# Optimization experiments

Measured on AMD Instinct MI355X. Metric: run time of the kernel, lower is better.

Reference implementation:

```python
import jax, jax.numpy as jnp
import numpy as np

# Config matching init_kwargs (single TP rank: local heads == total heads)
HID = 1024
NH = 16      # query heads
NKV = 4      # kv heads (GQA)
HD = 64      # head_dim
B = 2
S = 2048
SCALE = 1.0 / HD ** 0.5


def setup_inputs() -> dict:
    key = jax.random.key(0)
    k1, k2, k3 = jax.random.split(key, 3)
    qkv_out = (NH + 2 * NKV) * HD  # 1536
    return {
        "hidden_states": jax.random.normal(k1, (B, S, HID), dtype=jnp.float32),
        "W_qkv": jax.random.normal(k2, (HID, qkv_out), dtype=jnp.float32) * 0.02,
        "W_o": jax.random.normal(k3, (HID, HID), dtype=jnp.float32) * 0.02,
    }


def reference(hidden_states, W_qkv, W_o):
    b, s, _ = hidden_states.shape
    rep = NH // NKV  # GQA repeat factor (repeat_interleave: q head h uses kv group h // rep)

    qkv = hidden_states @ W_qkv  # [B, S, (NH+2*NKV)*HD]
    q, k, v = jnp.split(qkv, [NH * HD, (NH + NKV) * HD], axis=-1)

    # [B, heads, S, HD]
    q = q.reshape(b, s, NH, HD).transpose(0, 2, 1, 3)
    k = k.reshape(b, s, NKV, HD).transpose(0, 2, 1, 3)
    v = v.reshape(b, s, NKV, HD).transpose(0, 2, 1, 3)

    # Group query heads by shared kv head instead of repeat_interleaving K/V in memory.
    qg = q.reshape(b, NKV, rep, s, HD)  # head h = g*rep + r  <=>  kv group g = h // rep
    scores = jnp.einsum("bgrqd,bgkd->bgrqk", qg, k) * SCALE  # [B, NKV, rep, S, S]

    # Causal mask (prefill path: kv_cache is None, seq_len > 1)
    causal = jnp.triu(jnp.ones((s, s), dtype=bool), k=1)
    scores = jnp.where(causal, jnp.finfo(scores.dtype).min, scores)

    attn = jax.nn.softmax(scores, axis=-1)
    out = jnp.einsum("bgrqk,bgkd->bgrqd", attn, v)  # [B, NKV, rep, S, HD]
    out = out.reshape(b, NH, s, HD).transpose(0, 2, 1, 3).reshape(b, s, NH * HD)
    return out @ W_o  # [B, S, HID]
```

## Files before the change

### kernel.cpp

```cpp
#include <hip/hip_runtime.h>
#include <stdint.h>

using u16 = unsigned short;
using u32 = unsigned int;

typedef __attribute__((ext_vector_type(8))) short short8;
typedef __attribute__((ext_vector_type(4))) float f32x4;
typedef __attribute__((ext_vector_type(16))) float f32x16;

__device__ __forceinline__ u16 f2bf(float f) {
  u32 u = __builtin_bit_cast(u32, f);
  u = (u + 0x7fffu + ((u >> 16) & 1u)) >> 16;
  return (u16)u;
}

__device__ __forceinline__ u32 cvtpk(float lo, float hi) {
  u32 r;
  asm("v_cvt_pk_bf16_f32 %0, %1, %2" : "=v"(r) : "v"(lo), "v"(hi));
  return r;
}

__device__ __forceinline__ short8 ld16(const u16* p) {
  uint4 v = *(const uint4*)p;
  union { uint4 u; short8 s; } c; c.u = v; return c.s;
}

__device__ __forceinline__ void gload_lds16(const void* g, void* l) {
  __builtin_amdgcn_global_load_lds(
      (const __attribute__((address_space(1))) void*)g,
      (__attribute__((address_space(3))) void*)l, 16, 0, 0);
}

__device__ __forceinline__ f32x16 mfma32(short8 a, short8 b, f32x16 c) {
  return __builtin_amdgcn_mfma_f32_32x32x16_bf16(a, b, c, 0, 0, 0);
}

__global__ __launch_bounds__(256) void k_prep(const float* __restrict__ hs,
                                              const float* __restrict__ wqkv,
                                              const float* __restrict__ wo,
                                              u16* __restrict__ hsb,
                                              u16* __restrict__ wqkvT,
                                              u16* __restrict__ woT) {
  __shared__ float tile[32][33];
  const int bid = blockIdx.x;
  if (bid < 4096) {
    int i = bid * 256 + threadIdx.x;
    float4 v = ((const float4*)hs)[i];
    ushort4 o;
    o.x = f2bf(v.x); o.y = f2bf(v.y); o.z = f2bf(v.z); o.w = f2bf(v.w);
    ((ushort4*)hsb)[i] = o;
    return;
  }
  const float* in; u16* out; int R, C, bx, by;
  if (bid < 5632) {
    int idx = bid - 4096;
    in = wqkv; out = wqkvT; R = 1024; C = 1536;
    bx = idx % 48; by = idx / 48;
  } else {
    int idx = bid - 5632;
    in = wo; out = woT; R = 1024; C = 1024;
    bx = idx & 31; by = idx >> 5;
  }
  int c0 = bx * 32, r0 = by * 32;
  int tx = threadIdx.x & 31, ty = threadIdx.x >> 5;
#pragma unroll
  for (int i = 0; i < 4; ++i) {
    int r = ty + 8 * i;
    tile[r][tx] = in[(size_t)(r0 + r) * C + c0 + tx];
  }
  __syncthreads();
#pragma unroll
  for (int i = 0; i < 4; ++i) {
    int r = ty + 8 * i;
    out[(size_t)(c0 + r) * R + r0 + tx] = f2bf(tile[tx][r]);
  }
}

__global__ __launch_bounds__(256, 2) void k_gemm_qkv(
    const u16* __restrict__ A, const u16* __restrict__ BT,
    u16* __restrict__ qb, u16* __restrict__ kb, u16* __restrict__ vbT) {
  const int K = 1024, N = 1536;
  __shared__ __align__(16) u16 As[2][128 * 64];
  __shared__ __align__(16) u16 Bs[2][128 * 64];
  const int t = threadIdx.x;
  const int l = t & 63;
  const int wid = t >> 6;
  const int wr = wid >> 1, wc = wid & 1;
  const int lr = l & 15, lg = l >> 4;
  const int cpx = (int)gridDim.x >> 3;
  const int nb = (blockIdx.x & 7) * cpx + ((int)blockIdx.x >> 3);
  const int ntile = N >> 7;
  const int mt = nb / ntile, nt = nb % ntile;
  const int m0 = mt << 7, n0 = nt << 7;

  f32x4 zero = {0.f, 0.f, 0.f, 0.f};
  f32x4 acc[4][4];
#pragma unroll
  for (int i = 0; i < 4; ++i)
#pragma unroll
    for (int j = 0; j < 4; ++j) acc[i][j] = zero;

  const u16* Ab = A + (size_t)m0 * K;
  const u16* Bb = BT + (size_t)n0 * K;
  const int nkt = K >> 6;

  auto STAGE = [&](int kt, int bsel) {
    const u16* Ak = Ab + kt * 64;
    const u16* Bk = Bb + kt * 64;
#pragma unroll
    for (int i = 0; i < 4; ++i) {
      int o16 = i * 256 + t;
      int row = o16 >> 3, c = o16 & 7;
      int sc = c ^ (row & 7);
      gload_lds16(Ak + (size_t)row * K + sc * 8, &As[bsel][o16 * 8]);
    }
#pragma unroll
    for (int i = 0; i < 4; ++i) {
      int o16 = i * 256 + t;
      int row = o16 >> 3, c = o16 & 7;
      int sc = c ^ (row & 7);
      gload_lds16(Bk + (size_t)row * K + sc * 8, &Bs[bsel][o16 * 8]);
    }
  };

  STAGE(0, 0);
  asm volatile("s_waitcnt vmcnt(0)" ::: "memory");
  __builtin_amdgcn_s_barrier();

  for (int kt = 0; kt < nkt; ++kt) {
    const int cur = kt & 1;
    if (kt + 1 < nkt) STAGE(kt + 1, cur ^ 1);
#pragma unroll
    for (int ks = 0; ks < 2; ++ks) {
      short8 a[4], b[4];
#pragma unroll
      for (int mi = 0; mi < 4; ++mi) {
        int row = wr * 64 + mi * 16 + lr;
        int c = (ks * 4 + lg) ^ (row & 7);
        a[mi] = ld16(&As[cur][(row * 8 + c) * 8]);
      }
#pragma unroll
      for (int ni = 0; ni < 4; ++ni) {
        int row = wc * 64 + ni * 16 + lr;
        int c = (ks * 4 + lg) ^ (row & 7);
        b[ni] = ld16(&Bs[cur][(row * 8 + c) * 8]);
      }
#pragma unroll
      for (int mi = 0; mi < 4; ++mi)
#pragma unroll
        for (int ni = 0; ni < 4; ++ni)
          acc[mi][ni] = __builtin_amdgcn_mfma_f32_16x16x32_bf16(a[mi], b[ni], acc[mi][ni], 0, 0, 0);
    }
    asm volatile("s_waitcnt vmcnt(0)" ::: "memory");
    __builtin_amdgcn_s_barrier();
    asm volatile("" ::: "memory");
  }

#pragma unroll
  for (int mi = 0; mi < 4; ++mi) {
#pragma unroll
    for (int ni = 0; ni < 4; ++ni) {
#pragma unroll
      for (int r = 0; r < 4; ++r) {
        float v = acc[mi][ni][r];
        int m = m0 + wr * 64 + mi * 16 + 4 * lg + r;
        int n = n0 + wc * 64 + ni * 16 + lr;
        int bb = m >> 11, s = m & 2047;
        int tau = s >> 5, i32e = s & 31;
        if (n < 1024) {
          int h = n >> 6, d = n & 63;
          int kc = d >> 4, hi2 = (d >> 3) & 1, e = d & 7;
          qb[((size_t)(bb * 16 + h)) * 131072 +
             (size_t)((tau * 4 + kc) * 64 + (hi2 << 5 | i32e)) * 8 + e] = f2bf(v * 0.18033688f);
        } else if (n < 1280) {
          int g = (n - 1024) >> 6, d = n & 63;
          int kc = d >> 4, hi2 = (d >> 3) & 1, e = d & 7;
          kb[((size_t)(bb * 4 + g)) * 131072 +
             (size_t)((tau * 4 + kc) * 64 + (hi2 << 5 | i32e)) * 8 + e] = f2bf(v);
        } else {
          int g = (n - 1280) >> 6, dT = n & 63;
          int c = (s >> 4) & 1, hi2 = (s >> 3) & 1, e = s & 7;
          int dd = dT >> 5, i32v = dT & 31;
          vbT[((size_t)(bb * 4 + g)) * 131072 +
              (size_t)(((tau * 2 + dd) * 2 + c) * 64 + (hi2 << 5 | i32v)) * 8 + e] = f2bf(v);
        }
      }
    }
  }
}

__global__ __launch_bounds__(256, 2) void k_gemm_out(
    const u16* __restrict__ A, const u16* __restrict__ BT, float* __restrict__ out) {
  const int K = 1024, N = 1024;
  __shared__ __align__(16) u16 As[2][64 * 64];
  __shared__ __align__(16) u16 Bs[2][128 * 64];
  const int t = threadIdx.x;
  const int l = t & 63;
  const int wid = t >> 6;
  const int wr = wid >> 1, wc = wid & 1;
  const int lr = l & 15, lg = l >> 4;
  const int cpx = (int)gridDim.x >> 3;
  const int nb = (blockIdx.x & 7) * cpx + ((int)blockIdx.x >> 3);
  const int mt = nb >> 3, nt = nb & 7;
  const int m0 = mt << 6, n0 = nt << 7;

  f32x4 zero = {0.f, 0.f, 0.f, 0.f};
  f32x4 acc[2][4];
#pragma unroll
  for (int i = 0; i < 2; ++i)
#pragma unroll
    for (int j = 0; j < 4; ++j) acc[i][j] = zero;

  const u16* Ab = A + (size_t)m0 * K;
  const u16* Bb = BT + (size_t)n0 * K;

  auto STAGE = [&](int kt, int bsel) {
    const u16* Ak = Ab + kt * 64;
    const u16* Bk = Bb + kt * 64;
#pragma unroll
    for (int i = 0; i < 2; ++i) {
      int o16 = i * 256 + t;
      int row = o16 >> 3, c = o16 & 7;
      int sc = c ^ (row & 7);
      gload_lds16(Ak + (size_t)row * K + sc * 8, &As[bsel][o16 * 8]);
    }
#pragma unroll
    for (int i = 0; i < 4; ++i) {
      int o16 = i * 256 + t;
      int row = o16 >> 3, c = o16 & 7;
      int sc = c ^ (row & 7);
      gload_lds16(Bk + (size_t)row * K + sc * 8, &Bs[bsel][o16 * 8]);
    }
  };

  STAGE(0, 0);
  asm volatile("s_waitcnt vmcnt(0)" ::: "memory");
  __builtin_amdgcn_s_barrier();

  for (int kt = 0; kt < 16; ++kt) {
    const int cur = kt & 1;
    if (kt + 1 < 16) STAGE(kt + 1, cur ^ 1);
#pragma unroll
    for (int ks = 0; ks < 2; ++ks) {
      short8 a[2], b[4];
#pragma unroll
      for (int mi = 0; mi < 2; ++mi) {
        int row = wr * 32 + mi * 16 + lr;
        int c = (ks * 4 + lg) ^ (row & 7);
        a[mi] = ld16(&As[cur][(row * 8 + c) * 8]);
      }
#pragma unroll
      for (int ni = 0; ni < 4; ++ni) {
        int row = wc * 64 + ni * 16 + lr;
        int c = (ks * 4 + lg) ^ (row & 7);
        b[ni] = ld16(&Bs[cur][(row * 8 + c) * 8]);
      }
#pragma unroll
      for (int mi = 0; mi < 2; ++mi)
#pragma unroll
        for (int ni = 0; ni < 4; ++ni)
          acc[mi][ni] = __builtin_amdgcn_mfma_f32_16x16x32_bf16(a[mi], b[ni], acc[mi][ni], 0, 0, 0);
    }
    asm volatile("s_waitcnt vmcnt(0)" ::: "memory");
    __builtin_amdgcn_s_barrier();
    asm volatile("" ::: "memory");
  }

#pragma unroll
  for (int mi = 0; mi < 2; ++mi)
#pragma unroll
    for (int ni = 0; ni < 4; ++ni)
#pragma unroll
      for (int r = 0; r < 4; ++r) {
        int m = m0 + wr * 32 + mi * 16 + 4 * lg + r;
        int n = n0 + wc * 64 + ni * 16 + lr;
        out[(size_t)m * N + n] = acc[mi][ni][r];
      }
}

__global__ __launch_bounds__(256, 2) void k_attn(const u16* __restrict__ qbuf,
                                                 const u16* __restrict__ kbuf,
                                                 const u16* __restrict__ vbuf,
                                                 u16* __restrict__ attn) {
  const int t = threadIdx.x;
  const int l = t & 63, wid = t >> 6;
  const int i32 = l & 31, hi = l >> 5;
  const int bh = blockIdx.x >> 4;
  const int t16 = blockIdx.x & 15;
  const int b = bh >> 4, h = bh & 15, g = h >> 2;
  const int qt = (wid == 0) ? t16 : (wid == 1) ? 31 - t16 : (wid == 2) ? 32 + t16 : 63 - t16;
  const int q0 = qt * 32;
  const int nblk = (q0 >> 6) + 1;

  const u16* qp = qbuf + ((size_t)(b * 16 + h)) * 131072;
  const u16* kp = kbuf + ((size_t)(b * 4 + g)) * 131072;
  const u16* vp = vbuf + ((size_t)(b * 4 + g)) * 131072;

  short8 qf[4];
#pragma unroll
  for (int kc = 0; kc < 4; ++kc)
    qf[kc] = ld16(qp + ((size_t)((q0 >> 5) * 4 + kc) * 64 + l) * 8);

  f32x16 z16 = {0.f, 0.f, 0.f, 0.f, 0.f, 0.f, 0.f, 0.f,
                0.f, 0.f, 0.f, 0.f, 0.f, 0.f, 0.f, 0.f};
  f32x16 o[2];
  o[0] = z16; o[1] = z16;
  float lsum = 0.f;

  short8 kA[2][4], kB[2][4];

  auto LOADK = [&](short8(&kf)[2][4], int kv0) {
#pragma unroll
    for (int mf = 0; mf < 2; ++mf)
#pragma unroll
      for (int kc = 0; kc < 4; ++kc)
        kf[mf][kc] = ld16(kp + ((size_t)((((kv0 >> 5) + mf) * 4 + kc)) * 64 + l) * 8);
  };

  auto PROCESS = [&](short8(&kf)[2][4], short8(&kn)[2][4], bool pref, int kv0, bool last) {
    short8 vf[2][2][2];
#pragma unroll
    for (int mf = 0; mf < 2; ++mf)
#pragma unroll
      for (int dd = 0; dd < 2; ++dd)
#pragma unroll
        for (int c = 0; c < 2; ++c)
          vf[dd][mf][c] = ld16(vp + ((size_t)((((kv0 >> 5) + mf) * 2 + dd) * 2 + c) * 64 + l) * 8);

    f32x16 sc[2];
    __builtin_amdgcn_s_setprio(1);
    sc[0] = mfma32(kf[0][0], qf[0], z16);
    sc[1] = mfma32(kf[1][0], qf[0], z16);
#pragma unroll
    for (int kc = 1; kc < 4; ++kc) {
      sc[0] = mfma32(kf[0][kc], qf[kc], sc[0]);
      sc[1] = mfma32(kf[1][kc], qf[kc], sc[1]);
    }
    __builtin_amdgcn_s_setprio(0);

    if (pref) LOADK(kn, kv0 + 64);

    if (last) {
      const int iloc = (q0 - kv0) + i32;
#pragma unroll
      for (int mf = 0; mf < 2; ++mf)
#pragma unroll
        for (int R = 0; R < 16; ++R) {
          int j = 32 * mf + (R & 3) + 8 * (R >> 2) + 4 * hi;
          if (j > iloc) sc[mf][R] = -1e30f;
        }
    }

    float s0 = 0.f, s1 = 0.f, s2 = 0.f, s3 = 0.f;
#pragma unroll
    for (int mf = 0; mf < 2; ++mf)
#pragma unroll
      for (int R = 0; R < 16; R += 4) {
        float p0 = __builtin_amdgcn_exp2f(sc[mf][R]);
        float p1 = __builtin_amdgcn_exp2f(sc[mf][R + 1]);
        float p2 = __builtin_amdgcn_exp2f(sc[mf][R + 2]);
        float p3 = __builtin_amdgcn_exp2f(sc[mf][R + 3]);
        sc[mf][R] = p0; sc[mf][R + 1] = p1; sc[mf][R + 2] = p2; sc[mf][R + 3] = p3;
        s0 += p0; s1 += p1; s2 += p2; s3 += p3;
      }
    lsum += (s0 + s1) + (s2 + s3);

    short8 pb[2][2];
#pragma unroll
    for (int mf = 0; mf < 2; ++mf)
#pragma unroll
      for (int c = 0; c < 2; ++c) {
        union { u32 w[4]; short8 s8; } U;
#pragma unroll
        for (int q = 0; q < 2; ++q) {
          u32 wa = cvtpk(sc[mf][8 * c + 2 * q], sc[mf][8 * c + 2 * q + 1]);
          u32 wb = cvtpk(sc[mf][8 * c + 4 + 2 * q], sc[mf][8 * c + 4 + 2 * q + 1]);
          auto rr = __builtin_amdgcn_permlane32_swap(wa, wb, false, false);
          U.w[q] = (u32)rr[0];
          U.w[2 + q] = (u32)rr[1];
        }
        pb[mf][c] = U.s8;
      }

    __builtin_amdgcn_s_setprio(1);
#pragma unroll
    for (int mf = 0; mf < 2; ++mf)
#pragma unroll
      for (int c = 0; c < 2; ++c) {
        o[0] = mfma32(vf[0][mf][c], pb[mf][c], o[0]);
        o[1] = mfma32(vf[1][mf][c], pb[mf][c], o[1]);
      }
    __builtin_amdgcn_s_setprio(0);
  };

  LOADK(kA, 0);
  int kv0 = 0, blk = 0;
  while (true) {
    PROCESS(kA, kB, blk + 1 < nblk, kv0, blk == nblk - 1);
    ++blk; kv0 += 64;
    if (blk >= nblk) break;
    PROCESS(kB, kA, blk + 1 < nblk, kv0, blk == nblk - 1);
    ++blk; kv0 += 64;
    if (blk >= nblk) break;
  }

  float tot;
  {
    u32 su = __builtin_bit_cast(u32, lsum);
    auto rr = __builtin_amdgcn_permlane32_swap(su, su, false, false);
    tot = __builtin_bit_cast(float, (u32)rr[0]) + __builtin_bit_cast(float, (u32)rr[1]);
  }
  float inv = 1.f / tot;
  u16* ao = attn + ((size_t)(b * 2048 + q0)) * 1024 + h * 64;
#pragma unroll
  for (int dd = 0; dd < 2; ++dd) {
#pragma unroll
    for (int R = 0; R < 16; R += 2) {
      int d = dd * 32 + (R & 3) + 8 * (R >> 2) + 4 * hi;
      u32 w = cvtpk(o[dd][R] * inv, o[dd][R + 1] * inv);
      *(u32*)(ao + (size_t)i32 * 1024 + d) = w;
    }
  }
}

extern "C" void kernel_launch(void* const* d_in, const int* in_sizes, int n_in,
                              void* d_out, int out_size, void* d_ws, size_t ws_size,
                              hipStream_t stream) {
  const float* hs = (const float*)d_in[0];
  const float* wqkv = (const float*)d_in[1];
  const float* wo = (const float*)d_in[2];
  float* out = (float*)d_out;
  u16* ws = (u16*)d_ws;

  u16* hsb = ws;
  u16* wqkvT = hsb + 4194304;
  u16* woT = wqkvT + 1572864;
  u16* qb = woT + 1048576;
  u16* kb = qb + 4194304;
  u16* vb = kb + 1048576;
  u16* attn = vb + 1048576;
  (void)in_sizes; (void)n_in; (void)out_size; (void)ws_size;

  k_prep<<<6656, 256, 0, stream>>>(hs, wqkv, wo, hsb, wqkvT, woT);
  k_gemm_qkv<<<384, 256, 0, stream>>>(hsb, wqkvT, qb, kb, vb);
  k_attn<<<512, 256, 0, stream>>>(qb, kb, vb, attn);
  k_gemm_out<<<512, 256, 0, stream>>>(attn, woT, out);
}
```

Baseline: 85.14 us.

## Split attention KV range across waves and shrink QKV GEMM tiles

The attention kernel now assigns one 32-row query tile per block and splits its KV blocks across the four waves in strides of four. Partial outputs and row sums are combined through shared memory before the final normalize and store. This works without max-rescaling because the scores are unnormalized exp2 with no running max. The QKV GEMM halves its M tile to 64 so it launches twice as many blocks, and both kernels raise the occupancy hint to 3. The aim is better load balance and more blocks across CUs, at the cost of extra LDS traffic, a block barrier, and less per-block reuse in the GEMM.

```diff
diff --git a/kernel.cpp b/kernel.cpp
--- a/kernel.cpp
+++ b/kernel.cpp
@@ -76,11 +76,11 @@
   }
 }
 
-__global__ __launch_bounds__(256, 2) void k_gemm_qkv(
+__global__ __launch_bounds__(256, 3) void k_gemm_qkv(
     const u16* __restrict__ A, const u16* __restrict__ BT,
     u16* __restrict__ qb, u16* __restrict__ kb, u16* __restrict__ vbT) {
-  const int K = 1024, N = 1536;
-  __shared__ __align__(16) u16 As[2][128 * 64];
+  const int K = 1024;
+  __shared__ __align__(16) u16 As[2][64 * 64];
   __shared__ __align__(16) u16 Bs[2][128 * 64];
   const int t = threadIdx.x;
   const int l = t & 63;
@@ -89,26 +89,24 @@
   const int lr = l & 15, lg = l >> 4;
   const int cpx = (int)gridDim.x >> 3;
   const int nb = (blockIdx.x & 7) * cpx + ((int)blockIdx.x >> 3);
-  const int ntile = N >> 7;
-  const int mt = nb / ntile, nt = nb % ntile;
-  const int m0 = mt << 7, n0 = nt << 7;
+  const int mt = nb / 12, nt = nb % 12;
+  const int m0 = mt << 6, n0 = nt << 7;
 
   f32x4 zero = {0.f, 0.f, 0.f, 0.f};
-  f32x4 acc[4][4];
-#pragma unroll
-  for (int i = 0; i < 4; ++i)
+  f32x4 acc[2][4];
+#pragma unroll
+  for (int i = 0; i < 2; ++i)
 #pragma unroll
     for (int j = 0; j < 4; ++j) acc[i][j] = zero;
 
   const u16* Ab = A + (size_t)m0 * K;
   const u16* Bb = BT + (size_t)n0 * K;
-  const int nkt = K >> 6;
 
   auto STAGE = [&](int kt, int bsel) {
     const u16* Ak = Ab + kt * 64;
     const u16* Bk = Bb + kt * 64;
 #pragma unroll
-    for (int i = 0; i < 4; ++i) {
+    for (int i = 0; i < 2; ++i) {
       int o16 = i * 256 + t;
       int row = o16 >> 3, c = o16 & 7;
       int sc = c ^ (row & 7);
@@ -127,15 +125,15 @@
   asm volatile("s_waitcnt vmcnt(0)" ::: "memory");
   __builtin_amdgcn_s_barrier();
 
-  for (int kt = 0; kt < nkt; ++kt) {
+  for (int kt = 0; kt < 16; ++kt) {
     const int cur = kt & 1;
-    if (kt + 1 < nkt) STAGE(kt + 1, cur ^ 1);
+    if (kt + 1 < 16) STAGE(kt + 1, cur ^ 1);
 #pragma unroll
     for (int ks = 0; ks < 2; ++ks) {
-      short8 a[4], b[4];
-#pragma unroll
-      for (int mi = 0; mi < 4; ++mi) {
-        int row = wr * 64 + mi * 16 + lr;
+      short8 a[2], b[4];
+#pragma unroll
+      for (int mi = 0; mi < 2; ++mi) {
+        int row = wr * 32 + mi * 16 + lr;
         int c = (ks * 4 + lg) ^ (row & 7);
         a[mi] = ld16(&As[cur][(row * 8 + c) * 8]);
       }
@@ -146,7 +144,7 @@
         b[ni] = ld16(&Bs[cur][(row * 8 + c) * 8]);
       }
 #pragma unroll
-      for (int mi = 0; mi < 4; ++mi)
+      for (int mi = 0; mi < 2; ++mi)
 #pragma unroll
         for (int ni = 0; ni < 4; ++ni)
           acc[mi][ni] = __builtin_amdgcn_mfma_f32_16x16x32_bf16(a[mi], b[ni], acc[mi][ni], 0, 0, 0);
@@ -157,13 +155,13 @@
   }
 
 #pragma unroll
-  for (int mi = 0; mi < 4; ++mi) {
+  for (int mi = 0; mi < 2; ++mi) {
 #pragma unroll
     for (int ni = 0; ni < 4; ++ni) {
 #pragma unroll
       for (int r = 0; r < 4; ++r) {
         float v = acc[mi][ni][r];
-        int m = m0 + wr * 64 + mi * 16 + 4 * lg + r;
+        int m = m0 + wr * 32 + mi * 16 + 4 * lg + r;
         int n = n0 + wc * 64 + ni * 16 + lr;
         int bb = m >> 11, s = m & 2047;
         int tau = s >> 5, i32e = s & 31;
@@ -278,19 +276,20 @@
       }
 }
 
-__global__ __launch_bounds__(256, 2) void k_attn(const u16* __restrict__ qbuf,
+__global__ __launch_bounds__(256, 3) void k_attn(const u16* __restrict__ qbuf,
                                                  const u16* __restrict__ kbuf,
                                                  const u16* __restrict__ vbuf,
                                                  u16* __restrict__ attn) {
+  __shared__ float oshare[3 * 2048];
+  __shared__ float lshare[3 * 64];
   const int t = threadIdx.x;
   const int l = t & 63, wid = t >> 6;
   const int i32 = l & 31, hi = l >> 5;
-  const int bh = blockIdx.x >> 4;
-  const int t16 = blockIdx.x & 15;
+  const int bh = blockIdx.x >> 6;
+  const int qt = blockIdx.x & 63;
   const int b = bh >> 4, h = bh & 15, g = h >> 2;
-  const int qt = (wid == 0) ? t16 : (wid == 1) ? 31 - t16 : (wid == 2) ? 32 + t16 : 63 - t16;
   const int q0 = qt * 32;
-  const int nblk = (q0 >> 6) + 1;
+  const int nblk = (qt >> 1) + 1;
 
   const u16* qp = qbuf + ((size_t)(b * 16 + h)) * 131072;
   const u16* kp = kbuf + ((size_t)(b * 4 + g)) * 131072;
@@ -338,7 +337,7 @@
     }
     __builtin_amdgcn_s_setprio(0);
 
-    if (pref) LOADK(kn, kv0 + 64);
+    if (pref) LOADK(kn, kv0 + 256);
 
     if (last) {
       const int iloc = (q0 - kv0) + i32;
@@ -393,32 +392,64 @@
     __builtin_amdgcn_s_setprio(0);
   };
 
-  LOADK(kA, 0);
-  int kv0 = 0, blk = 0;
-  while (true) {
-    PROCESS(kA, kB, blk + 1 < nblk, kv0, blk == nblk - 1);
-    ++blk; kv0 += 64;
-    if (blk >= nblk) break;
-    PROCESS(kB, kA, blk + 1 < nblk, kv0, blk == nblk - 1);
-    ++blk; kv0 += 64;
-    if (blk >= nblk) break;
-  }
-
-  float tot;
-  {
-    u32 su = __builtin_bit_cast(u32, lsum);
-    auto rr = __builtin_amdgcn_permlane32_swap(su, su, false, false);
-    tot = __builtin_bit_cast(float, (u32)rr[0]) + __builtin_bit_cast(float, (u32)rr[1]);
-  }
-  float inv = 1.f / tot;
-  u16* ao = attn + ((size_t)(b * 2048 + q0)) * 1024 + h * 64;
-#pragma unroll
-  for (int dd = 0; dd < 2; ++dd) {
-#pragma unroll
-    for (int R = 0; R < 16; R += 2) {
-      int d = dd * 32 + (R & 3) + 8 * (R >> 2) + 4 * hi;
-      u32 w = cvtpk(o[dd][R] * inv, o[dd][R + 1] * inv);
-      *(u32*)(ao + (size_t)i32 * 1024 + d) = w;
+  if (wid < nblk) {
+    LOADK(kA, wid * 64);
+    int n = wid;
+    while (true) {
+      PROCESS(kA, kB, n + 4 < nblk, n * 64, n == nblk - 1);
+      n += 4; if (n >= nblk) break;
+      PROCESS(kB, kA, n + 4 < nblk, n * 64, n == nblk - 1);
+      n += 4; if (n >= nblk) break;
+    }
+  }
+
+  if (wid > 0) {
+    const int base = (wid - 1) * 2048;
+#pragma unroll
+    for (int dd = 0; dd < 2; ++dd) {
+      float4* dst = (float4*)&oshare[base + (dd * 64 + l) * 16];
+#pragma unroll
+      for (int q = 0; q < 4; ++q) {
+        float4 v4;
+        v4.x = o[dd][4 * q]; v4.y = o[dd][4 * q + 1];
+        v4.z = o[dd][4 * q + 2]; v4.w = o[dd][4 * q + 3];
+        dst[q] = v4;
+      }
+    }
+    lshare[(wid - 1) * 64 + l] = lsum;
+  }
+  __syncthreads();
+  if (wid == 0) {
+#pragma unroll
+    for (int w = 0; w < 3; ++w) {
+#pragma unroll
+      for (int dd = 0; dd < 2; ++dd) {
+        const float4* src = (const float4*)&oshare[w * 2048 + (dd * 64 + l) * 16];
+#pragma unroll
+        for (int q = 0; q < 4; ++q) {
+          float4 v4 = src[q];
+          o[dd][4 * q] += v4.x; o[dd][4 * q + 1] += v4.y;
+          o[dd][4 * q + 2] += v4.z; o[dd][4 * q + 3] += v4.w;
+        }
+      }
+      lsum += lshare[w * 64 + l];
+    }
+    float tot;
+    {
+      u32 su = __builtin_bit_cast(u32, lsum);
+      auto rr = __builtin_amdgcn_permlane32_swap(su, su, false, false);
+      tot = __builtin_bit_cast(float, (u32)rr[0]) + __builtin_bit_cast(float, (u32)rr[1]);
+    }
+    float inv = 1.f / tot;
+    u16* ao = attn + ((size_t)(b * 2048 + q0)) * 1024 + h * 64;
+#pragma unroll
+    for (int dd = 0; dd < 2; ++dd) {
+#pragma unroll
+      for (int R = 0; R < 16; R += 2) {
+        int d = dd * 32 + (R & 3) + 8 * (R >> 2) + 4 * hi;
+        u32 w = cvtpk(o[dd][R] * inv, o[dd][R + 1] * inv);
+        *(u32*)(ao + (size_t)i32 * 1024 + d) = w;
+      }
     }
   }
 }
@@ -442,7 +473,7 @@
   (void)in_sizes; (void)n_in; (void)out_size; (void)ws_size;
 
   k_prep<<<6656, 256, 0, stream>>>(hs, wqkv, wo, hsb, wqkvT, woT);
-  k_gemm_qkv<<<384, 256, 0, stream>>>(hsb, wqkvT, qb, kb, vb);
-  k_attn<<<512, 256, 0, stream>>>(qb, kb, vb, attn);
+  k_gemm_qkv<<<768, 256, 0, stream>>>(hsb, wqkvT, qb, kb, vb);
+  k_attn<<<2048, 256, 0, stream>>>(qb, kb, vb, attn);
   k_gemm_out<<<512, 256, 0, stream>>>(attn, woT, out);
 }
```

Result: slower. 228.2 us (+168.0%).
